# Optimization experiments

Hardware: AMD Instinct MI355X
Metric: run time of the kernel (lower is better)

The kernel has to match this reference:

```python
import jax, jax.numpy as jnp
import numpy as np

B = 256          # graphs per batch
NPG = 512        # nodes per graph (equal-size AIGs)
N = B * NPG      # 131072 total nodes
E = 2 * N        # AIG: ~2 fanins per AND node
H = 256          # hidden_channels
EMB = 3          # node-type embedding dim
IN = EMB + 1     # node_encoder_out_channels


def _p(k, shape, fan_in):
    return jax.random.normal(k, shape, jnp.float32) / np.float32(np.sqrt(fan_in))


def setup_inputs():
    key = jax.random.key(0)
    ks = list(jax.random.split(key, 24))
    nt = jax.random.randint(ks[0], (N, 1), 0, 3)
    ninv = jax.random.randint(ks[1], (N, 1), 0, 3)
    x = jnp.concatenate([nt, ninv], axis=1).astype(jnp.int32)
    # within-graph random edges
    epg = E // B
    gid = jnp.repeat(jnp.arange(B), epg)
    src = gid * NPG + jax.random.randint(ks[2], (E,), 0, NPG)
    dst = gid * NPG + jax.random.randint(ks[3], (E,), 0, NPG)
    edge_index = jnp.stack([src, dst]).astype(jnp.int32)
    batch = jnp.repeat(jnp.arange(B), NPG).astype(jnp.int32)
    d = dict(x=x, edge_index=edge_index, batch=batch)
    d['emb_w'] = _p(ks[4], (3, EMB), 1)
    d['c1_lW'] = _p(ks[5], (IN, H), IN); d['c1_lb'] = jnp.zeros((H,), jnp.float32)
    d['c1_rW'] = _p(ks[6], (IN, H), IN)
    d['t1'] = jnp.float32(0.1)
    d['c2_lW'] = _p(ks[7], (H, H), H); d['c2_lb'] = jnp.zeros((H,), jnp.float32)
    d['c2_rW'] = _p(ks[8], (H, H), H)
    d['t2'] = jnp.float32(0.1)
    d['mlp_W'] = _p(ks[9], (NPG * H, H), NPG * H); d['mlp_b'] = jnp.zeros((H,), jnp.float32)
    d['gru_Wih'] = _p(ks[10], (3 * H, H), H); d['gru_Whh'] = _p(ks[11], (3 * H, H), H)
    d['gru_bih'] = jnp.zeros((3 * H,), jnp.float32); d['gru_bhh'] = jnp.zeros((3 * H,), jnp.float32)
    d['st_Wq'] = _p(ks[12], (3, H, H), H); d['st_bq'] = jnp.zeros((3, H), jnp.float32)
    d['st_Wk'] = _p(ks[13], (3, H, H), H); d['st_bk'] = jnp.zeros((3, H), jnp.float32)
    d['st_Wv'] = _p(ks[14], (3, H, H), H); d['st_bv'] = jnp.zeros((3, H), jnp.float32)
    d['st_Wo'] = _p(ks[15], (3, H, H), H); d['st_bo'] = jnp.zeros((3, H), jnp.float32)
    d['st_lW'] = _p(ks[16], (3, H, H), H); d['st_lb'] = jnp.zeros((3, H), jnp.float32)
    d['pma_lW'] = _p(ks[17], (H, H), H); d['pma_lb'] = jnp.zeros((H,), jnp.float32)
    d['seed'] = _p(ks[18], (1, H), H)
    d['fin_W'] = _p(ks[19], (3 * H, 3 * H), 3 * H); d['fin_b'] = jnp.zeros((3 * H,), jnp.float32)
    return d


def _softmax_aggr(msg, idx, t, n):
    # PyG SoftmaxAggregation: alpha = softmax(msg * t per target segment); sum(msg * alpha)
    logits = msg * t                                   # [E, C]
    m = jax.ops.segment_max(logits, idx, num_segments=n)
    m = jnp.where(jnp.isfinite(m), m, 0.0)             # empty segments -> 0
    ex = jnp.exp(logits - m[idx])
    s = jax.ops.segment_sum(ex, idx, num_segments=n)
    alpha = ex / s[idx]
    return jax.ops.segment_sum(msg * alpha, idx, num_segments=n)


def _sage(h, edge_index, lW, lb, rW, t):
    # SAGEConv: lin_l(softmax_aggr(x_j -> i)) + lin_r(x_i)
    msg = h[edge_index[0]]                             # gather sources [E, C]
    ag = _softmax_aggr(msg, edge_index[1], t, N)       # scatter-softmax-scatter
    return ag @ lW + lb + h @ rW


def _gru_last(xd, Wih, Whh, bih, bhh):
    # torch GRU over [B, T, H]; return last output
    def step(h, x_t):
        gi = x_t @ Wih.T + bih
        gh = h @ Whh.T + bhh
        ir, iz, inn = jnp.split(gi, 3, axis=-1)
        hr, hz, hn = jnp.split(gh, 3, axis=-1)
        r = jax.nn.sigmoid(ir + hr)
        z = jax.nn.sigmoid(iz + hz)
        nn_ = jnp.tanh(inn + r * hn)
        h_new = (1.0 - z) * nn_ + z * h
        return h_new, None
    h0 = jnp.zeros((xd.shape[0], H), xd.dtype)
    hT, _ = jax.lax.scan(step, h0, jnp.swapaxes(xd, 0, 1))
    return hT


def _mab(q, k, Wq, bq, Wk, bk, Wv, bv, Wo, bo, Wl, bl):
    # Set-Transformer MAB, 1 head, no layer norm (PyG defaults)
    Q = q @ Wq + bq
    K = k @ Wk + bk
    V = k @ Wv + bv
    A = jax.nn.softmax(jnp.einsum('bqd,bkd->bqk', Q, K) / np.float32(np.sqrt(H)), axis=-1)
    h = q + (jnp.einsum('bqk,bkd->bqd', A, V) @ Wo + bo)
    return h + jax.nn.relu(h @ Wl + bl)


def _set_transformer(xd, Wq, bq, Wk, bk, Wv, bv, Wo, bo, Wl, bl, pma_lW, pma_lb, seed):
    def mab_i(i, q, k):
        return _mab(q, k, Wq[i], bq[i], Wk[i], bk[i], Wv[i], bv[i], Wo[i], bo[i], Wl[i], bl[i])
    h = mab_i(0, xd, xd)                               # encoder SAB [B, NPG, H]
    kk = jax.nn.relu(h @ pma_lW + pma_lb)
    s = jnp.broadcast_to(seed[None], (xd.shape[0], 1, H))
    s = mab_i(1, s, kk)                                # PMA (1 seed)
    s = mab_i(2, s, s)                                 # decoder SAB
    return s.reshape(xd.shape[0], H)


def _forward(x, edge_index, batch, emb_w, c1_lW, c1_lb, c1_rW, t1, c2_lW, c2_lb, c2_rW, t2,
             mlp_W, mlp_b, gru_Wih, gru_Whh, gru_bih, gru_bhh,
             st_Wq, st_bq, st_Wk, st_bk, st_Wv, st_bv, st_Wo, st_bo, st_lW, st_lb,
             pma_lW, pma_lb, seed, fin_W, fin_b):
    # NodeEncoder: embed node_type, concat num_inverted_predecessors as float
    h = jnp.concatenate([emb_w[x[:, 0]], x[:, 1:2].astype(jnp.float32)], axis=1)  # [N, 4]
    h = jax.nn.relu(_sage(h, edge_index, c1_lW, c1_lb, c1_rW, t1))
    h = jax.nn.relu(_sage(h, edge_index, c2_lW, c2_lb, c2_rW, t2))
    # equal-size sorted graphs -> dense batch is a reshape
    xd = h.reshape(B, NPG, H)
    p1 = xd.reshape(B, NPG * H) @ mlp_W + mlp_b                       # MLPAggregation
    p2 = _gru_last(xd, gru_Wih, gru_Whh, gru_bih, gru_bhh)            # GRUAggregation
    p3 = _set_transformer(xd, st_Wq, st_bq, st_Wk, st_bk, st_Wv, st_bv,
                          st_Wo, st_bo, st_lW, st_lb, pma_lW, pma_lb, seed)
    pooled = jnp.concatenate([p1, p2, p3], axis=1)                    # [B, 3H]
    return pooled @ fin_W + fin_b


def reference(x, edge_index, batch, emb_w, c1_lW, c1_lb, c1_rW, t1, c2_lW, c2_lb, c2_rW, t2,
              mlp_W, mlp_b, gru_Wih, gru_Whh, gru_bih, gru_bhh,
              st_Wq, st_bq, st_Wk, st_bk, st_Wv, st_bv, st_Wo, st_bo, st_lW, st_lb,
              pma_lW, pma_lb, seed, fin_W, fin_b):
    return _forward(x, edge_index, batch, emb_w, c1_lW, c1_lb, c1_rW, t1, c2_lW, c2_lb, c2_rW, t2,
                    mlp_W, mlp_b, gru_Wih, gru_Whh, gru_bih, gru_bhh,
                    st_Wq, st_bq, st_Wk, st_bk, st_Wv, st_bv, st_Wo, st_bo, st_lW, st_lb,
                    pma_lW, pma_lb, seed, fin_W, fin_b)
```

## Files before the change

### kernel.cpp

```cpp
#include <hip/hip_runtime.h>
#include <hip/hip_bf16.h>
#include <math.h>

constexpr int NN   = 131072;
constexpr int NE   = 262144;
constexpr int BG   = 256;

typedef __bf16 bf16x8 __attribute__((ext_vector_type(8)));
typedef float  f32x4  __attribute__((ext_vector_type(4)));
typedef int    i32x4  __attribute__((ext_vector_type(4)));

__device__ inline float sigm(float x){ return 1.f/(1.f+__expf(-x)); }
__device__ inline unsigned short f2bu(float f){
  union{float f;unsigned u;}v; v.f=f;
  unsigned u = v.u + 0x7fffu + ((v.u>>16)&1u);
  return (unsigned short)(u>>16);
}
__device__ inline bf16x8 cvt8(float4 a, float4 b){
  union { ushort u[8]; bf16x8 v; } r;
  r.u[0]=f2bu(a.x); r.u[1]=f2bu(a.y); r.u[2]=f2bu(a.z); r.u[3]=f2bu(a.w);
  r.u[4]=f2bu(b.x); r.u[5]=f2bu(b.y); r.u[6]=f2bu(b.z); r.u[7]=f2bu(b.w);
  return r.v;
}

__global__ void k_zero(int* __restrict__ p, int n){
  int i = blockIdx.x*256 + threadIdx.x;
  if (i < n) p[i] = 0;
}

__global__ void k_node_enc(const int* __restrict__ x, const float* __restrict__ emb,
                           float* __restrict__ h0){
  int n = blockIdx.x*256 + threadIdx.x;
  if (n >= NN) return;
  int nt = x[2*n], ninv = x[2*n+1];
  float4 v; v.x = emb[nt*3+0]; v.y = emb[nt*3+1]; v.z = emb[nt*3+2]; v.w = (float)ninv;
  reinterpret_cast<float4*>(h0)[n] = v;
}

__global__ void k_count(const int* __restrict__ ei, int* __restrict__ deg){
  int e = blockIdx.x*256 + threadIdx.x;
  if (e >= NE) return;
  atomicAdd(&deg[ei[NE + e]], 1);
}
__global__ void k_blocksum(const int* __restrict__ deg, int* __restrict__ bsum){
  __shared__ int sd[256];
  int t = threadIdx.x;
  const int* p = deg + blockIdx.x*1024;
  int s = p[t*4] + p[t*4+1] + p[t*4+2] + p[t*4+3];
  sd[t]=s; __syncthreads();
  for (int d=128; d>0; d>>=1){ if (t<d) sd[t]+=sd[t+d]; __syncthreads(); }
  if (!t) bsum[blockIdx.x] = sd[0];
}
__global__ void k_scanbsum(const int* __restrict__ bsum, int* __restrict__ boff, int* __restrict__ offN){
  __shared__ int s[128];
  int t = threadIdx.x;
  int mine = bsum[t];
  s[t]=mine; __syncthreads();
  for (int d=1; d<128; d<<=1){ int v = (t>=d)? s[t-d]:0; __syncthreads(); s[t]+=v; __syncthreads(); }
  boff[t] = s[t]-mine;
  if (t==127) offN[0] = s[127];
}
__global__ void k_scanchunk(const int* __restrict__ deg, const int* __restrict__ boff, int* __restrict__ offs){
  __shared__ int ts[256];
  int t = threadIdx.x, b = blockIdx.x;
  const int* p = deg + b*1024;
  int v0=p[t*4],v1=p[t*4+1],v2=p[t*4+2],v3=p[t*4+3];
  int mysum=v0+v1+v2+v3;
  ts[t]=mysum; __syncthreads();
  for (int d=1; d<256; d<<=1){ int v=(t>=d)?ts[t-d]:0; __syncthreads(); ts[t]+=v; __syncthreads(); }
  int ex = ts[t]-mysum + boff[b];
  int* o = offs + b*1024 + t*4;
  o[0]=ex; o[1]=ex+v0; o[2]=ex+v0+v1; o[3]=ex+v0+v1+v2;
}
__global__ void k_fill(const int* __restrict__ ei, const int* __restrict__ offs,
                       int* __restrict__ cur, int* __restrict__ esrc){
  int e = blockIdx.x*256 + threadIdx.x;
  if (e >= NE) return;
  int dst = ei[NE+e];
  int pos = offs[dst] + atomicAdd(&cur[dst],1);
  esrc[pos] = ei[e];
}

__global__ void k_aggr4(const float* __restrict__ h, const int* __restrict__ offs,
                        const int* __restrict__ esrc, const float* __restrict__ tptr,
                        float* __restrict__ ag){
  int n = blockIdx.x*256 + threadIdx.x;
  if (n >= NN) return;
  int s = offs[n], e = offs[n+1];
  float4 z = {0,0,0,0};
  if (s == e){ reinterpret_cast<float4*>(ag)[n] = z; return; }
  float t = *tptr;
  float4 num=z, den=z;
  for (int i=s;i<e;++i){
    float4 v = reinterpret_cast<const float4*>(h)[esrc[i]];
    float ex;
    ex=__expf(v.x*t); num.x+=v.x*ex; den.x+=ex;
    ex=__expf(v.y*t); num.y+=v.y*ex; den.y+=ex;
    ex=__expf(v.z*t); num.z+=v.z*ex; den.z+=ex;
    ex=__expf(v.w*t); num.w+=v.w*ex; den.w+=ex;
  }
  float4 r = {num.x/den.x, num.y/den.y, num.z/den.z, num.w/den.w};
  reinterpret_cast<float4*>(ag)[n] = r;
}

__global__ __launch_bounds__(256) void k_aggr256(float* __restrict__ buf, const int* __restrict__ offs,
                          const int* __restrict__ esrc, const float* __restrict__ tptr, int base){
  int n = base + blockIdx.x, c = threadIdx.x;
  int s = offs[n], e = offs[n+1];
  float* outp = buf + (size_t)blockIdx.x*512 + 256 + c;
  if (s == e){ *outp = 0.f; return; }
  float t = *tptr;
  float num=0.f, den=0.f;
  for (int i=s;i<e;++i){
    float v = buf[(size_t)(esrc[i]-base)*512 + c];
    float ex = __expf(v*t);
    num += v*ex; den += ex;
  }
  *outp = num/den;
}

__global__ __launch_bounds__(256) void k_conv1_lin(const float* __restrict__ ag, const float* __restrict__ h0,
                            const float* __restrict__ lW, const float* __restrict__ lb,
                            const float* __restrict__ rW, float* __restrict__ out, int base){
  int n = base + blockIdx.x, c = threadIdx.x;
  float4 a  = reinterpret_cast<const float4*>(ag)[n];
  float4 xv = reinterpret_cast<const float4*>(h0)[n];
  float acc = lb[c];
  acc += a.x*lW[c]  + a.y*lW[256+c]  + a.z*lW[512+c]  + a.w*lW[768+c];
  acc += xv.x*rW[c] + xv.y*rW[256+c] + xv.z*rW[512+c] + xv.w*rW[768+c];
  out[(size_t)blockIdx.x*512 + c] = fmaxf(acc, 0.f);
}

#define GF_BIAS    1
#define GF_RELU    2
#define GF_RESID   4
#define GF_RESID_B 8
#define GF_ADDC    32
#define GF_ATOMIC  64
#define GF_BF16    128
#define GF_VTP     256

__global__ void k_packb(const float* __restrict__ W, ushort* __restrict__ Bp, int K, int N){
  int idx = blockIdx.x*256 + threadIdx.x;
  if (idx >= K*N) return;
  int k = idx / N, j = idx - k*N;
  Bp[((size_t)(k>>3)*N + j)*8 + (k&7)] = f2bu(W[idx]);
}
__global__ void k_packbT(const float* __restrict__ W, ushort* __restrict__ Bp, int K, int N){
  int idx = blockIdx.x*256 + threadIdx.x;
  if (idx >= K*N) return;
  int j = idx / K, k = idx - j*K;
  Bp[((size_t)(k>>3)*N + j)*8 + (k&7)] = f2bu(W[idx]);
}
__global__ __launch_bounds__(256) void k_packhh8(const float* __restrict__ gWhh,
                        char* __restrict__ Bp8, float* __restrict__ cs){
  int j = blockIdx.x, k = threadIdx.x;
  float w = gWhh[(size_t)j*256 + k];
  __shared__ float red[256];
  red[k] = fabsf(w); __syncthreads();
  for (int d=128; d>0; d>>=1){ if (k<d) red[k]=fmaxf(red[k],red[k+d]); __syncthreads(); }
  float mx = fmaxf(red[0], 1e-20f);
  int q = (int)lrintf(w * (127.f/mx));
  q = max(-127, min(127, q));
  Bp8[((size_t)(k>>3)*768 + j)*8 + (k&7)] = (char)q;
  if (k==0) cs[j] = mx/(127.f*127.f);
}
__global__ void k_packbias(const float* __restrict__ gbih, const float* __restrict__ gbhh,
                           float* __restrict__ bc){
  int i = blockIdx.x*256 + threadIdx.x;
  if (i >= 1024) return;
  int c = i & 255;
  float v;
  if (i < 256)      v = gbih[c] + gbhh[c];
  else if (i < 512) v = gbih[256+c] + gbhh[256+c];
  else if (i < 768) v = gbih[512+c];
  else              v = gbhh[512+c];
  bc[i] = v;
}

template<int FLAGS>
__global__ __launch_bounds__(256) void k_bgemm(const float* __restrict__ A, const ushort* __restrict__ Bp,
                       const float* __restrict__ bias, const float* __restrict__ resid,
                       float* __restrict__ C, int M, int Nn, int K, int lda){
  const int tid = threadIdx.x;
  const int wv = tid>>6, lane = tid&63;
  const int mw = wv>>1, nw = wv&1;
  const int arow = lane&15, ks = lane>>4;
  const int m0 = blockIdx.x*128 + mw*64, n0 = blockIdx.y*128 + nw*64;
  const int kChunk = K / gridDim.z, kBeg = blockIdx.z * kChunk;
  f32x4 acc[4][4] = {};
  const float* Arow0 = A + (size_t)(m0 + 0*16 + arow)*lda;
  const float* Arow1 = A + (size_t)(m0 + 1*16 + arow)*lda;
  const float* Arow2 = A + (size_t)(m0 + 2*16 + arow)*lda;
  const float* Arow3 = A + (size_t)(m0 + 3*16 + arow)*lda;
  #pragma unroll 2
  for (int k0 = kBeg; k0 < kBeg+kChunk; k0 += 32){
    const int kb = (k0>>3) + ks;
    bf16x8 af[4];
    {
      const float4* p0 = reinterpret_cast<const float4*>(Arow0 + k0 + ks*8);
      const float4* p1 = reinterpret_cast<const float4*>(Arow1 + k0 + ks*8);
      const float4* p2 = reinterpret_cast<const float4*>(Arow2 + k0 + ks*8);
      const float4* p3 = reinterpret_cast<const float4*>(Arow3 + k0 + ks*8);
      af[0] = cvt8(p0[0], p0[1]);
      af[1] = cvt8(p1[0], p1[1]);
      af[2] = cvt8(p2[0], p2[1]);
      af[3] = cvt8(p3[0], p3[1]);
    }
    #pragma unroll
    for (int nf=0; nf<4; ++nf){
      const int col = n0 + nf*16 + arow;
      bf16x8 bfr = *reinterpret_cast<const bf16x8*>(Bp + ((size_t)kb*Nn + col)*8);
      #pragma unroll
      for (int mf=0; mf<4; ++mf)
        acc[mf][nf] = __builtin_amdgcn_mfma_f32_16x16x32_bf16(af[mf], bfr, acc[mf][nf], 0, 0, 0);
    }
  }
  #pragma unroll
  for (int nf=0; nf<4; ++nf){
    const int n = n0 + nf*16 + arow;
    float bv  = (FLAGS & GF_BIAS)    ? bias[n]  : 0.f;
    float rbv = (FLAGS & GF_RESID_B) ? resid[n] : 0.f;
    #pragma unroll
    for (int mf=0; mf<4; ++mf){
      #pragma unroll
      for (int r=0; r<4; ++r){
        const int m = m0 + mf*16 + ks*4 + r;
        size_t idx = (size_t)m*Nn + n;
        float v = acc[mf][nf][r];
        if (FLAGS & GF_ATOMIC){ atomicAdd(&C[idx], v); }
        else {
          v += bv;
          if (FLAGS & GF_ADDC)  v += C[idx];
          if (FLAGS & GF_RELU)  v = fmaxf(v, 0.f);
          if (FLAGS & GF_RESID) v += resid[idx];
          v += rbv;
          if (FLAGS & GF_VTP){
            const int rr = m & 511, mg = m >> 9;
            ((ushort*)C)[(size_t)mg*131072 + (((rr>>3)*256 + n)<<3) + (rr&7)] = f2bu(v);
          }
          else if (FLAGS & GF_BF16) reinterpret_cast<__hip_bfloat16*>(C)[idx] = __float2bfloat16(v);
          else C[idx] = v;
        }
      }
    }
  }
}

__global__ __launch_bounds__(256) void k_qk(const float* __restrict__ Q, const ushort* __restrict__ Kb,
                                            float* __restrict__ S){
  const int tid = threadIdx.x;
  const int wv = tid>>6, lane = tid&63;
  const int mw = wv>>1, nw = wv&1;
  const int arow = lane&15, ks = lane>>4;
  const int m0 = blockIdx.x*128 + mw*64;
  const int n0 = blockIdx.y*128 + nw*64;
  const int g  = blockIdx.x>>2;
  const ushort* Kg = Kb + (size_t)g*131072;
  f32x4 acc[4][4] = {};
  const float* Ar0 = Q + (size_t)(m0 + 0*16 + arow)*256;
  const float* Ar1 = Q + (size_t)(m0 + 1*16 + arow)*256;
  const float* Ar2 = Q + (size_t)(m0 + 2*16 + arow)*256;
  const float* Ar3 = Q + (size_t)(m0 + 3*16 + arow)*256;
  #pragma unroll
  for (int k0 = 0; k0 < 256; k0 += 32){
    bf16x8 af[4];
    {
      const float4* p0 = reinterpret_cast<const float4*>(Ar0 + k0 + ks*8);
      const float4* p1 = reinterpret_cast<const float4*>(Ar1 + k0 + ks*8);
      const float4* p2 = reinterpret_cast<const float4*>(Ar2 + k0 + ks*8);
      const float4* p3 = reinterpret_cast<const float4*>(Ar3 + k0 + ks*8);
      af[0] = cvt8(p0[0], p0[1]);
      af[1] = cvt8(p1[0], p1[1]);
      af[2] = cvt8(p2[0], p2[1]);
      af[3] = cvt8(p3[0], p3[1]);
    }
    #pragma unroll
    for (int nf=0; nf<4; ++nf){
      const int j = n0 + nf*16 + arow;
      bf16x8 bfr = *reinterpret_cast<const bf16x8*>(Kg + (size_t)j*256 + k0 + ks*8);
      #pragma unroll
      for (int mf=0; mf<4; ++mf)
        acc[mf][nf] = __builtin_amdgcn_mfma_f32_16x16x32_bf16(af[mf], bfr, acc[mf][nf], 0, 0, 0);
    }
  }
  #pragma unroll
  for (int nf=0; nf<4; ++nf){
    const int n = n0 + nf*16 + arow;
    #pragma unroll
    for (int mf=0; mf<4; ++mf){
      #pragma unroll
      for (int r=0; r<4; ++r){
        const int m = m0 + mf*16 + ks*4 + r;
        S[(size_t)m*512 + n] = acc[mf][nf][r];
      }
    }
  }
}

__global__ __launch_bounds__(256) void k_smrow(const float* __restrict__ S, ushort* __restrict__ P){
  const int row = blockIdx.x, tid = threadIdx.x;
  __shared__ float red[4];
  const float* sr = S + (size_t)row*512;
  float s0 = sr[tid], s1 = sr[tid+256];
  float m = fmaxf(s0, s1);
  #pragma unroll
  for (int o=1;o<64;o<<=1) m = fmaxf(m, __shfl_xor(m,o));
  if ((tid&63)==0) red[tid>>6] = m;
  __syncthreads();
  m = fmaxf(fmaxf(red[0],red[1]), fmaxf(red[2],red[3]));
  __syncthreads();
  float e0 = __expf((s0-m)*0.0625f), e1 = __expf((s1-m)*0.0625f);
  float s = e0+e1;
  #pragma unroll
  for (int o=1;o<64;o<<=1) s += __shfl_xor(s,o);
  if ((tid&63)==0) red[tid>>6] = s;
  __syncthreads();
  s = red[0]+red[1]+red[2]+red[3];
  float inv = 1.f/s;
  P[(size_t)row*512 + tid]       = f2bu(e0*inv);
  P[(size_t)row*512 + 256 + tid] = f2bu(e1*inv);
}

__global__ __launch_bounds__(256) void k_av(const ushort* __restrict__ Pb, const ushort* __restrict__ VTp,
                                            float* __restrict__ O){
  const int tid = threadIdx.x;
  const int wv = tid>>6, lane = tid&63;
  const int mw = wv>>1, nw = wv&1;
  const int arow = lane&15, ks = lane>>4;
  const int m0 = blockIdx.x*128 + mw*64;
  const int n0 = blockIdx.y*128 + nw*64;
  const int g  = blockIdx.x>>2;
  const ushort* Vg = VTp + (size_t)g*131072;
  f32x4 acc[4][4] = {};
  const ushort* Pr0 = Pb + (size_t)(m0 + 0*16 + arow)*512;
  const ushort* Pr1 = Pb + (size_t)(m0 + 1*16 + arow)*512;
  const ushort* Pr2 = Pb + (size_t)(m0 + 2*16 + arow)*512;
  const ushort* Pr3 = Pb + (size_t)(m0 + 3*16 + arow)*512;
  #pragma unroll 2
  for (int k0 = 0; k0 < 512; k0 += 32){
    const int kb = (k0>>3) + ks;
    bf16x8 af[4];
    af[0] = *reinterpret_cast<const bf16x8*>(Pr0 + k0 + ks*8);
    af[1] = *reinterpret_cast<const bf16x8*>(Pr1 + k0 + ks*8);
    af[2] = *reinterpret_cast<const bf16x8*>(Pr2 + k0 + ks*8);
    af[3] = *reinterpret_cast<const bf16x8*>(Pr3 + k0 + ks*8);
    #pragma unroll
    for (int nf=0; nf<4; ++nf){
      const int col = n0 + nf*16 + arow;
      bf16x8 bfr = *reinterpret_cast<const bf16x8*>(Vg + ((size_t)kb*256 + col)*8);
      #pragma unroll
      for (int mf=0; mf<4; ++mf)
        acc[mf][nf] = __builtin_amdgcn_mfma_f32_16x16x32_bf16(af[mf], bfr, acc[mf][nf], 0, 0, 0);
    }
  }
  #pragma unroll
  for (int nf=0; nf<4; ++nf){
    const int n = n0 + nf*16 + arow;
    #pragma unroll
    for (int mf=0; mf<4; ++mf){
      #pragma unroll
      for (int r=0; r<4; ++r){
        const int m = m0 + mf*16 + ks*4 + r;
        O[(size_t)m*256 + n] = acc[mf][nf][r];
      }
    }
  }
}

__global__ void k_rowbias(const float* __restrict__ bias, float* __restrict__ C, int Nn, int total){
  int i = blockIdx.x*256 + threadIdx.x;
  if (i < total) C[i] = bias[i % Nn];
}
__global__ void k_qvec(const float* __restrict__ seed, const float* __restrict__ Wq,
                       const float* __restrict__ bq, float* __restrict__ qv){
  __shared__ float s[256];
  int t = threadIdx.x;
  s[t] = seed[t]; __syncthreads();
  float acc = bq[t];
  for (int c = 0; c < 256; ++c) acc += s[c] * Wq[c*256 + t];
  qv[t] = acc;
}
__global__ __launch_bounds__(256) void k_wk2q(const float* __restrict__ Wk2, const float* __restrict__ bk2,
                      const float* __restrict__ qv, float* __restrict__ outv){
  __shared__ float qs[256];
  __shared__ float red[4];
  int t = threadIdx.x;
  qs[t] = qv[t]; __syncthreads();
  float a = 0.f;
  for (int c=0;c<256;c+=4){
    float4 w = *reinterpret_cast<const float4*>(Wk2 + t*256 + c);
    a += w.x*qs[c] + w.y*qs[c+1] + w.z*qs[c+2] + w.w*qs[c+3];
  }
  outv[t] = a;
  float bb = bk2[t]*qs[t];
  #pragma unroll
  for (int o=1;o<64;o<<=1) bb += __shfl_xor(bb,o);
  if ((t&63)==0) red[t>>6] = bb;
  __syncthreads();
  if (t==0) outv[256] = red[0]+red[1]+red[2]+red[3];
}
__global__ __launch_bounds__(256) void k_pmafuse(const float* __restrict__ kk, const float* __restrict__ wkq,
                        float* __restrict__ wsum){
  int g = blockIdx.x, tid = threadIdx.x;
  __shared__ float qs[256];
  __shared__ float sc[512];
  __shared__ float red[4];
  qs[tid] = wkq[tid];
  __syncthreads();
  const float b2q = wkq[256];
  const float* kg = kk + (size_t)g*512*256;
  float l0=0.f, l1=0.f;
  for (int j0=0;j0<2;++j0){
    int j = tid + j0*256;
    const float* kr = kg + (size_t)j*256;
    float a = 0.f;
    for (int c=0;c<256;c+=4){
      float4 k4 = *reinterpret_cast<const float4*>(kr + c);
      a += k4.x*qs[c] + k4.y*qs[c+1] + k4.z*qs[c+2] + k4.w*qs[c+3];
    }
    a = (a + b2q)*0.0625f;
    if (j0) l1=a; else l0=a;
  }
  float m = fmaxf(l0,l1);
  #pragma unroll
  for (int o=1;o<64;o<<=1) m = fmaxf(m, __shfl_xor(m,o));
  if ((tid&63)==0) red[tid>>6] = m;
  __syncthreads();
  m = fmaxf(fmaxf(red[0],red[1]), fmaxf(red[2],red[3]));
  __syncthreads();
  float e0 = __expf(l0-m), e1 = __expf(l1-m);
  sc[tid]=e0; sc[tid+256]=e1;
  float s = e0+e1;
  #pragma unroll
  for (int o=1;o<64;o<<=1) s += __shfl_xor(s,o);
  if ((tid&63)==0) red[tid>>6] = s;
  __syncthreads();
  s = red[0]+red[1]+red[2]+red[3];
  float invs = 1.f/s;
  float acc = 0.f;
  for (int j=0;j<512;++j) acc += sc[j] * kg[(size_t)j*256 + tid];
  wsum[(size_t)g*256+tid] = acc*invs;
}
__global__ void k_concat(const float* __restrict__ p1, const float* __restrict__ p2,
                         const float* __restrict__ p3, float* __restrict__ pooled){
  int idx = blockIdx.x*256 + threadIdx.x;
  int b = idx / 768, j = idx % 768;
  float v = (j < 256) ? p1[b*256+j] : (j < 512) ? p2[b*256+j-256] : p3[b*256+j-512];
  pooled[idx] = v;
}

__global__ __launch_bounds__(512) void k_gru10(const float* __restrict__ X,
                      const ushort* __restrict__ pIh, const char* __restrict__ pHh8,
                      const float* __restrict__ csg, const float* __restrict__ bc,
                      float* __restrict__ p2){
  extern __shared__ char gsm[];
  float*  GIw  = (float*)gsm;
  float*  gh   = (float*)(gsm + 98304);
  float*  bcl  = (float*)(gsm + 101376);
  float*  csl  = (float*)(gsm + 105472);
  char*   hbf8 = (char*) (gsm + 108544);
  const int g = blockIdx.x;
  const int tid = threadIdx.x;
  const int wv = tid>>6, lane = tid&63;
  const int arow = lane&15, ks = lane>>4;
  for (int i=tid;i<1024;i+=512) bcl[i] = bc[i];
  for (int i=tid;i<768;i+=512)  csl[i] = csg[i];
  if (tid < 256) hbf8[tid] = 0;
  float h_reg = 0.f;
  const float* Xg = X + (size_t)g*512*256;
  __syncthreads();
  for (int w=0; w<16; ++w){
    const int t0 = w*32;
    #pragma unroll
    for (int mt=0; mt<2; ++mt){
      const float* xr = Xg + (size_t)(t0 + mt*16 + arow)*256;
      f32x4 acc[6] = {};
      #pragma unroll
      for (int kt=0; kt<8; ++kt){
        const float4* xp = reinterpret_cast<const float4*>(xr + kt*32 + ks*8);
        bf16x8 af = cvt8(xp[0], xp[1]);
        #pragma unroll
        for (int nt=0; nt<6; ++nt){
          bf16x8 bfr = *reinterpret_cast<const bf16x8*>(pIh + ((size_t)(kt*4+ks)*768 + wv*96+nt*16+arow)*8);
          acc[nt] = __builtin_amdgcn_mfma_f32_16x16x32_bf16(af, bfr, acc[nt], 0,0,0);
        }
      }
      #pragma unroll
      for (int nt=0; nt<6; ++nt){
        const int col = wv*96 + nt*16 + arow;
        #pragma unroll
        for (int r=0;r<4;++r)
          GIw[(size_t)(mt*16 + ks*4 + r)*768 + col] = acc[nt][r];
      }
    }
    for (int dt=0; dt<32; ++dt){
      i32x4 sacc[6] = {};
      #pragma unroll
      for (int kt=0; kt<8; ++kt){
        long a8 = 0;
        if (arow == 0) a8 = *reinterpret_cast<const long*>(hbf8 + kt*32 + ks*8);
        #pragma unroll
        for (int nt=0; nt<6; ++nt){
          const int col = wv*96 + nt*16 + arow;
          long b8 = *reinterpret_cast<const long*>(pHh8 + ((size_t)(kt*4+ks)*768 + col)*8);
          sacc[nt] = __builtin_amdgcn_mfma_i32_16x16x32_i8(a8, b8, sacc[nt], 0,0,0);
        }
      }
      if (ks == 0){
        #pragma unroll
        for (int nt=0; nt<6; ++nt){
          const int col = wv*96 + nt*16 + arow;
          gh[col] = (float)sacc[nt][0] * csl[col];
        }
      }
      __syncthreads();
      if (tid < 256){
        const int c = tid;
        const float* gir = GIw + (size_t)dt*768;
        float rr = sigm(gir[c]     + gh[c]     + bcl[c]);
        float zz = sigm(gir[256+c] + gh[256+c] + bcl[256+c]);
        float nn = tanhf(gir[512+c] + bcl[512+c] + rr*(gh[512+c] + bcl[768+c]));
        h_reg = (1.f-zz)*nn + zz*h_reg;
        int q = (int)lrintf(h_reg*127.f);
        q = max(-127, min(127, q));
        hbf8[c] = (char)q;
      }
      __syncthreads();
    }
  }
  if (tid < 256) p2[(size_t)g*256 + tid] = h_reg;
}

extern "C" void kernel_launch(void* const* d_in, const int* in_sizes, int n_in,
                              void* d_out, int out_size, void* d_ws, size_t ws_size,
                              hipStream_t stream){
  const int*   x      = (const int*)  d_in[0];
  const int*   ei     = (const int*)  d_in[1];
  const float* emb_w  = (const float*)d_in[3];
  const float* c1_lW  = (const float*)d_in[4];
  const float* c1_lb  = (const float*)d_in[5];
  const float* c1_rW  = (const float*)d_in[6];
  const float* t1     = (const float*)d_in[7];
  const float* c2_lW  = (const float*)d_in[8];
  const float* c2_lb  = (const float*)d_in[9];
  const float* c2_rW  = (const float*)d_in[10];
  const float* t2     = (const float*)d_in[11];
  const float* mlp_W  = (const float*)d_in[12];
  const float* mlp_b  = (const float*)d_in[13];
  const float* gWih   = (const float*)d_in[14];
  const float* gWhh   = (const float*)d_in[15];
  const float* gbih   = (const float*)d_in[16];
  const float* gbhh   = (const float*)d_in[17];
  const float* stWq   = (const float*)d_in[18];
  const float* stbq   = (const float*)d_in[19];
  const float* stWk   = (const float*)d_in[20];
  const float* stbk   = (const float*)d_in[21];
  const float* stWv   = (const float*)d_in[22];
  const float* stbv   = (const float*)d_in[23];
  const float* stWo   = (const float*)d_in[24];
  const float* stbo   = (const float*)d_in[25];
  const float* stlW   = (const float*)d_in[26];
  const float* stlb   = (const float*)d_in[27];
  const float* pma_lW = (const float*)d_in[28];
  const float* pma_lb = (const float*)d_in[29];
  const float* seed   = (const float*)d_in[30];
  const float* fin_W  = (const float*)d_in[31];
  const float* fin_b  = (const float*)d_in[32];
  float* out = (float*)d_out;

  auto needFor = [](int CHe)->size_t{
    size_t bufN = (size_t)CHe*512*512;
    size_t floats = (size_t)33554432 + 3*bufN + 2*524288 + 2*196608 + 8*65536 + 196608 + 320 + 512;
    size_t ints   = 131072 + 131200 + 131072 + 262144 + 128 + 128;
    return floats*4 + ints*4 + 4096;
  };
  const int CHe = (ws_size >= needFor(64)) ? 64 : 32;
  if (ws_size < needFor(32)) return;
  const int NCHUNKe = BG / CHe;
  const int NCNe = CHe * 512;
  const size_t bufN = (size_t)CHe*512*512;

  float* H2   = (float*)d_ws;
  float* bufA = H2   + (size_t)33554432;
  float* bufB = bufA + bufN;
  float* bufC = bufB + bufN;
  float* h0   = bufC + bufN;
  float* ag1  = h0   + (size_t)524288;
  float* wT1  = ag1  + (size_t)524288;
  float* wT2  = wT1  + (size_t)196608;
  float* p1   = wT2  + (size_t)196608;
  float* p2   = p1   + (size_t)65536;
  float* p3   = p2   + (size_t)65536;
  float* av2  = p3   + (size_t)65536;
  float* s1   = av2  + (size_t)65536;
  float* s2v  = s1   + (size_t)65536;
  float* v3   = s2v  + (size_t)65536;
  float* h3   = v3   + (size_t)65536;
  float* pooled = h3 + (size_t)65536;
  float* qv   = pooled + (size_t)196608;
  int*   deg  = (int*)(qv + 320);
  int*   offs = deg  + 131072;
  int*   cur  = offs + 131200;
  int*   esrc = cur  + 131072;
  int*   bsum = esrc + 262144;
  int*   boff = bsum + 128;
  float* wkq  = (float*)(boff + 128);

  ushort* pIh  = (ushort*)wT1;
  char*   pHh8 = (char*)(wT1 + 98304);
  float*  csHh = wT1 + 98304 + 49152;
  ushort* pC2  = (ushort*)wT2;
  float*  bcomb= wT2 + 65536;
  float*  pa   = h0;
  ushort* pQ0  = (ushort*)(pa);
  ushort* pK0  = (ushort*)(pa + 32768);
  ushort* pV0  = (ushort*)(pa + 65536);
  ushort* pO0  = (ushort*)(pa + 98304);
  ushort* pL0  = (ushort*)(pa + 131072);
  ushort* pPma = (ushort*)(pa + 163840);
  ushort* pV1  = (ushort*)(pa + 229376);
  ushort* pO1  = (ushort*)(pa + 262144);
  ushort* pL1  = (ushort*)(pa + 294912);
  ushort* pV2  = (ushort*)(pa + 327680);
  ushort* pO2  = (ushort*)(pa + 360448);
  ushort* pL2  = (ushort*)(pa + 393216);
  ushort* pFin = (ushort*)(pa + 425984);

  ushort* VTp = (ushort*)(bufA + bufN/2);
  ushort* Kbf = (ushort*)bufB;
  ushort* Pbf = (ushort*)(bufB + bufN/4);

  const int ls0 = 65536, ls1 = 256;

  k_node_enc<<<NN/256, 256, 0, stream>>>(x, emb_w, h0);

  k_zero<<<NN/256, 256, 0, stream>>>(deg, NN);
  k_count<<<NE/256, 256, 0, stream>>>(ei, deg);
  k_blocksum<<<128, 256, 0, stream>>>(deg, bsum);
  k_scanbsum<<<1, 128, 0, stream>>>(bsum, boff, offs + NN);
  k_scanchunk<<<128, 256, 0, stream>>>(deg, boff, offs);
  k_zero<<<NN/256, 256, 0, stream>>>(cur, NN);
  k_fill<<<NE/256, 256, 0, stream>>>(ei, offs, cur, esrc);

  k_aggr4<<<NN/256, 256, 0, stream>>>(h0, offs, esrc, t1, ag1);
  k_packb <<<256, 256, 0, stream>>>(c2_rW, pC2, 256, 256);
  k_packb <<<256, 256, 0, stream>>>(c2_lW, pC2 + 65536, 256, 256);
  k_packbT<<<768, 256, 0, stream>>>(gWih, pIh, 256, 768);
  k_packhh8<<<768, 256, 0, stream>>>(gWhh, pHh8, csHh);
  k_packbias<<<4, 256, 0, stream>>>(gbih, gbhh, bcomb);

  for (int cg = 0; cg < NCHUNKe; ++cg){
    const int base = cg * NCNe;
    float* Hc = H2 + (size_t)base * 256;
    const dim3 gg(NCNe/128, 2, 1);
    k_conv1_lin<<<NCNe, 256, 0, stream>>>(ag1, h0, c1_lW, c1_lb, c1_rW, bufA, base);
    k_aggr256<<<NCNe, 256, 0, stream>>>(bufA, offs, esrc, t2, base);
    k_bgemm<GF_BIAS|GF_RELU><<<gg, 256, 0, stream>>>(bufA, pC2, c2_lb, nullptr, Hc, NCNe, 256, 512, 512);
  }

  k_packb<<<131072, 256, 0, stream>>>(mlp_W, (ushort*)bufB, 131072, 256);
  k_rowbias<<<256, 256, 0, stream>>>(mlp_b, p1, 256, 65536);
  k_bgemm<GF_ATOMIC><<<dim3(2, 2, 64), 256, 0, stream>>>(H2, (ushort*)bufB, nullptr, nullptr, p1, 256, 256, NN, 131072);

  k_gru10<<<BG, 512, 108800, stream>>>(H2, pIh, pHh8, csHh, bcomb, p2);

  k_packb<<<256, 256, 0, stream>>>(stWq,        pQ0, 256, 256);
  k_packb<<<256, 256, 0, stream>>>(stWk,        pK0, 256, 256);
  k_packb<<<256, 256, 0, stream>>>(stWv,        pV0, 256, 256);
  k_packb<<<256, 256, 0, stream>>>(stWo,        pO0, 256, 256);
  k_packb<<<256, 256, 0, stream>>>(stlW,        pL0, 256, 256);
  k_packb<<<256, 256, 0, stream>>>(pma_lW,      pPma,256, 256);
  k_packb<<<256, 256, 0, stream>>>(stWv + ls0,  pV1, 256, 256);
  k_packb<<<256, 256, 0, stream>>>(stWo + ls0,  pO1, 256, 256);
  k_packb<<<256, 256, 0, stream>>>(stlW + ls0,  pL1, 256, 256);
  k_packb<<<256, 256, 0, stream>>>(stWv + 2*ls0,pV2, 256, 256);
  k_packb<<<256, 256, 0, stream>>>(stWo + 2*ls0,pO2, 256, 256);
  k_packb<<<256, 256, 0, stream>>>(stlW + 2*ls0,pL2, 256, 256);
  k_packb<<<2304, 256, 0, stream>>>(fin_W,      pFin,768, 768);
  k_qvec<<<1, 256, 0, stream>>>(seed, stWq + ls0, stbq + ls1, qv);
  k_wk2q<<<1, 256, 0, stream>>>(stWk + ls0, stbk + ls1, qv, wkq);

  for (int cg = 0; cg < NCHUNKe; ++cg){
    const int base = cg * NCNe;
    float* Hc = H2 + (size_t)base * 256;
    const dim3 gg(NCNe/128, 2, 1);
    k_bgemm<GF_BIAS><<<gg, 256, 0, stream>>>(Hc, pQ0, stbq, nullptr, bufA, NCNe, 256, 256, 256);
    k_bgemm<GF_BIAS|GF_BF16><<<gg, 256, 0, stream>>>(Hc, pK0, stbk, nullptr, (float*)Kbf, NCNe, 256, 256, 256);
    k_bgemm<GF_BIAS|GF_VTP><<<gg, 256, 0, stream>>>(Hc, pV0, stbv, nullptr, (float*)VTp, NCNe, 256, 256, 256);
    k_qk<<<dim3(NCNe/128, 4), 256, 0, stream>>>(bufA, Kbf, bufC);
    k_smrow<<<NCNe, 256, 0, stream>>>(bufC, Pbf);
    k_av<<<dim3(NCNe/128, 2), 256, 0, stream>>>(Pbf, VTp, bufA);
    k_bgemm<GF_BIAS|GF_RESID><<<gg, 256, 0, stream>>>(bufA, pO0, stbo, Hc, Hc, NCNe, 256, 256, 256);
    k_bgemm<GF_BIAS|GF_RELU|GF_RESID><<<gg, 256, 0, stream>>>(Hc, pL0, stlb, Hc, bufA, NCNe, 256, 256, 256);
    k_bgemm<GF_BIAS|GF_RELU><<<gg, 256, 0, stream>>>(bufA, pPma, pma_lb, nullptr, bufB, NCNe, 256, 256, 256);
    k_pmafuse<<<CHe, 256, 0, stream>>>(bufB, wkq, av2 + (size_t)cg*CHe*256);
  }

  k_bgemm<GF_BIAS><<<dim3(2, 2, 1), 256, 0, stream>>>(av2, pV1, stbv + ls1, nullptr, v3, 256, 256, 256, 256);
  k_bgemm<GF_BIAS|GF_RESID_B><<<dim3(2, 2, 1), 256, 0, stream>>>(v3, pO1, stbo + ls1, seed, s1, 256, 256, 256, 256);
  k_bgemm<GF_BIAS|GF_RELU|GF_RESID><<<dim3(2, 2, 1), 256, 0, stream>>>(s1, pL1, stlb + ls1, s1, s2v, 256, 256, 256, 256);
  k_bgemm<GF_BIAS><<<dim3(2, 2, 1), 256, 0, stream>>>(s2v, pV2, stbv + 2*ls1, nullptr, v3, 256, 256, 256, 256);
  k_bgemm<GF_BIAS|GF_RESID><<<dim3(2, 2, 1), 256, 0, stream>>>(v3, pO2, stbo + 2*ls1, s2v, h3, 256, 256, 256, 256);
  k_bgemm<GF_BIAS|GF_RELU|GF_RESID><<<dim3(2, 2, 1), 256, 0, stream>>>(h3, pL2, stlb + 2*ls1, h3, p3, 256, 256, 256, 256);

  k_concat<<<768, 256, 0, stream>>>(p1, p2, p3, pooled);
  k_bgemm<GF_BIAS><<<dim3(2, 6, 1), 256, 0, stream>>>(pooled, pFin, fin_b, nullptr, out, 256, 768, 768, 768);
}
```

Before: 3.152 ms.

## Store node activations and attention intermediates in bf16, widen GEMM tiles

The conv2 output H2 and the set-transformer intermediates (Q, attention output, residual stream, PMA keys) are now stored as bf16 instead of fp32. Downstream GEMMs load bf16 fragments directly instead of converting fp32, and the GRU, MLP split-K and PMA kernels read bf16 too. A new GEMM kernel covers all 256 output columns per block with wider N tiles, and GRU tanh is replaced by an exp-based fast form. This halves activation memory traffic and conversion work, at the cost of extra rounding, since the residual stream is now accumulated in bf16.

```diff
diff --git a/kernel.cpp b/kernel.cpp
--- a/kernel.cpp
+++ b/kernel.cpp
@@ -11,6 +11,9 @@
 typedef int    i32x4  __attribute__((ext_vector_type(4)));
 
 __device__ inline float sigm(float x){ return 1.f/(1.f+__expf(-x)); }
+__device__ inline float blo(unsigned u){ union{unsigned a;float f;}v; v.a=u<<16; return v.f; }
+__device__ inline float bhi(unsigned u){ union{unsigned a;float f;}v; v.a=u&0xffff0000u; return v.f; }
+__device__ inline float b2f(ushort u){ union{unsigned a;float f;}v; v.a=((unsigned)u)<<16; return v.f; }
 __device__ inline unsigned short f2bu(float f){
   union{float f;unsigned u;}v; v.f=f;
   unsigned u = v.u + 0x7fffu + ((v.u>>16)&1u);
@@ -139,6 +142,7 @@
 #define GF_ATOMIC  64
 #define GF_BF16    128
 #define GF_VTP     256
+#define GF_RESID16 512
 
 __global__ void k_packb(const float* __restrict__ W, ushort* __restrict__ Bp, int K, int N){
   int idx = blockIdx.x*256 + threadIdx.x;
@@ -187,25 +191,15 @@
   const int mw = wv>>1, nw = wv&1;
   const int arow = lane&15, ks = lane>>4;
   const int m0 = blockIdx.x*128 + mw*64, n0 = blockIdx.y*128 + nw*64;
-  const int kChunk = K / gridDim.z, kBeg = blockIdx.z * kChunk;
   f32x4 acc[4][4] = {};
-  const float* Arow0 = A + (size_t)(m0 + 0*16 + arow)*lda;
-  const float* Arow1 = A + (size_t)(m0 + 1*16 + arow)*lda;
-  const float* Arow2 = A + (size_t)(m0 + 2*16 + arow)*lda;
-  const float* Arow3 = A + (size_t)(m0 + 3*16 + arow)*lda;
   #pragma unroll 2
-  for (int k0 = kBeg; k0 < kBeg+kChunk; k0 += 32){
+  for (int k0 = 0; k0 < K; k0 += 32){
     const int kb = (k0>>3) + ks;
     bf16x8 af[4];
-    {
-      const float4* p0 = reinterpret_cast<const float4*>(Arow0 + k0 + ks*8);
-      const float4* p1 = reinterpret_cast<const float4*>(Arow1 + k0 + ks*8);
-      const float4* p2 = reinterpret_cast<const float4*>(Arow2 + k0 + ks*8);
-      const float4* p3 = reinterpret_cast<const float4*>(Arow3 + k0 + ks*8);
-      af[0] = cvt8(p0[0], p0[1]);
-      af[1] = cvt8(p1[0], p1[1]);
-      af[2] = cvt8(p2[0], p2[1]);
-      af[3] = cvt8(p3[0], p3[1]);
+    #pragma unroll
+    for (int mf=0; mf<4; ++mf){
+      const float4* p = reinterpret_cast<const float4*>(A + (size_t)(m0+mf*16+arow)*lda + k0 + ks*8);
+      af[mf] = cvt8(p[0], p[1]);
     }
     #pragma unroll
     for (int nf=0; nf<4; ++nf){
@@ -228,27 +222,86 @@
         const int m = m0 + mf*16 + ks*4 + r;
         size_t idx = (size_t)m*Nn + n;
         float v = acc[mf][nf][r];
-        if (FLAGS & GF_ATOMIC){ atomicAdd(&C[idx], v); }
+        v += bv;
+        if (FLAGS & GF_RELU)  v = fmaxf(v, 0.f);
+        if (FLAGS & GF_RESID) v += resid[idx];
+        v += rbv;
+        C[idx] = v;
+      }
+    }
+  }
+}
+
+template<int FLAGS, bool ABF>
+__global__ __launch_bounds__(256) void k_bgemm2(const void* __restrict__ Av, const ushort* __restrict__ Bp,
+                       const float* __restrict__ bias, const void* __restrict__ residv,
+                       void* __restrict__ Cv, int K, int lda){
+  const int tid = threadIdx.x;
+  const int wv = tid>>6, lane = tid&63;
+  const int mw = wv&1, nw = wv>>1;
+  const int arow = lane&15, ks = lane>>4;
+  const int m0 = blockIdx.x*128 + mw*64;
+  const int n0 = nw*128;
+  const int kChunk = K / gridDim.z, kBeg = blockIdx.z * kChunk;
+  f32x4 acc[4][8] = {};
+  #pragma unroll 1
+  for (int k0 = kBeg; k0 < kBeg+kChunk; k0 += 32){
+    const int kb = (k0>>3) + ks;
+    bf16x8 af[4];
+    if (ABF){
+      const ushort* A = (const ushort*)Av;
+      #pragma unroll
+      for (int mf=0; mf<4; ++mf)
+        af[mf] = *reinterpret_cast<const bf16x8*>(A + (size_t)(m0+mf*16+arow)*lda + k0 + ks*8);
+    } else {
+      const float* A = (const float*)Av;
+      #pragma unroll
+      for (int mf=0; mf<4; ++mf){
+        const float4* p = reinterpret_cast<const float4*>(A + (size_t)(m0+mf*16+arow)*lda + k0 + ks*8);
+        af[mf] = cvt8(p[0], p[1]);
+      }
+    }
+    #pragma unroll
+    for (int nf=0; nf<8; ++nf){
+      const int col = n0 + nf*16 + arow;
+      bf16x8 bfr = *reinterpret_cast<const bf16x8*>(Bp + ((size_t)kb*256 + col)*8);
+      #pragma unroll
+      for (int mf=0; mf<4; ++mf)
+        acc[mf][nf] = __builtin_amdgcn_mfma_f32_16x16x32_bf16(af[mf], bfr, acc[mf][nf], 0, 0, 0);
+    }
+  }
+  #pragma unroll
+  for (int nf=0; nf<8; ++nf){
+    const int n = n0 + nf*16 + arow;
+    float bv = (FLAGS & GF_BIAS) ? bias[n] : 0.f;
+    #pragma unroll
+    for (int mf=0; mf<4; ++mf){
+      #pragma unroll
+      for (int r=0; r<4; ++r){
+        const int m = m0 + mf*16 + ks*4 + r;
+        size_t idx = (size_t)m*256 + n;
+        float v = acc[mf][nf][r];
+        if (FLAGS & GF_ATOMIC){ atomicAdd((float*)Cv + idx, v); }
         else {
           v += bv;
-          if (FLAGS & GF_ADDC)  v += C[idx];
-          if (FLAGS & GF_RELU)  v = fmaxf(v, 0.f);
-          if (FLAGS & GF_RESID) v += resid[idx];
-          v += rbv;
+          if (FLAGS & GF_RELU) v = fmaxf(v, 0.f);
+          if (FLAGS & GF_RESID16) v += b2f(((const ushort*)residv)[idx]);
           if (FLAGS & GF_VTP){
             const int rr = m & 511, mg = m >> 9;
-            ((ushort*)C)[(size_t)mg*131072 + (((rr>>3)*256 + n)<<3) + (rr&7)] = f2bu(v);
+            ((ushort*)Cv)[(size_t)mg*131072 + (((rr>>3)*256 + n)<<3) + (rr&7)] = f2bu(v);
+          } else if (FLAGS & GF_BF16){
+            ((ushort*)Cv)[idx] = f2bu(v);
+          } else {
+            ((float*)Cv)[idx] = v;
           }
-          else if (FLAGS & GF_BF16) reinterpret_cast<__hip_bfloat16*>(C)[idx] = __float2bfloat16(v);
-          else C[idx] = v;
         }
       }
     }
   }
 }
 
-__global__ __launch_bounds__(256) void k_qk(const float* __restrict__ Q, const ushort* __restrict__ Kb,
-                                            float* __restrict__ S){
+__global__ __launch_bounds__(256) void k_qk16(const ushort* __restrict__ Qb, const ushort* __restrict__ Kb,
+                                              float* __restrict__ S){
   const int tid = threadIdx.x;
   const int wv = tid>>6, lane = tid&63;
   const int mw = wv>>1, nw = wv&1;
@@ -258,23 +311,12 @@
   const int g  = blockIdx.x>>2;
   const ushort* Kg = Kb + (size_t)g*131072;
   f32x4 acc[4][4] = {};
-  const float* Ar0 = Q + (size_t)(m0 + 0*16 + arow)*256;
-  const float* Ar1 = Q + (size_t)(m0 + 1*16 + arow)*256;
-  const float* Ar2 = Q + (size_t)(m0 + 2*16 + arow)*256;
-  const float* Ar3 = Q + (size_t)(m0 + 3*16 + arow)*256;
   #pragma unroll
   for (int k0 = 0; k0 < 256; k0 += 32){
     bf16x8 af[4];
-    {
-      const float4* p0 = reinterpret_cast<const float4*>(Ar0 + k0 + ks*8);
-      const float4* p1 = reinterpret_cast<const float4*>(Ar1 + k0 + ks*8);
-      const float4* p2 = reinterpret_cast<const float4*>(Ar2 + k0 + ks*8);
-      const float4* p3 = reinterpret_cast<const float4*>(Ar3 + k0 + ks*8);
-      af[0] = cvt8(p0[0], p0[1]);
-      af[1] = cvt8(p1[0], p1[1]);
-      af[2] = cvt8(p2[0], p2[1]);
-      af[3] = cvt8(p3[0], p3[1]);
-    }
+    #pragma unroll
+    for (int mf=0; mf<4; ++mf)
+      af[mf] = *reinterpret_cast<const bf16x8*>(Qb + (size_t)(m0+mf*16+arow)*256 + k0 + ks*8);
     #pragma unroll
     for (int nf=0; nf<4; ++nf){
       const int j = n0 + nf*16 + arow;
@@ -322,31 +364,26 @@
   P[(size_t)row*512 + 256 + tid] = f2bu(e1*inv);
 }
 
-__global__ __launch_bounds__(256) void k_av(const ushort* __restrict__ Pb, const ushort* __restrict__ VTp,
-                                            float* __restrict__ O){
+__global__ __launch_bounds__(256) void k_av2(const ushort* __restrict__ Pb, const ushort* __restrict__ VTp,
+                                             ushort* __restrict__ Ob){
   const int tid = threadIdx.x;
   const int wv = tid>>6, lane = tid&63;
-  const int mw = wv>>1, nw = wv&1;
+  const int mw = wv&1, nw = wv>>1;
   const int arow = lane&15, ks = lane>>4;
   const int m0 = blockIdx.x*128 + mw*64;
-  const int n0 = blockIdx.y*128 + nw*64;
+  const int n0 = nw*128;
   const int g  = blockIdx.x>>2;
   const ushort* Vg = VTp + (size_t)g*131072;
-  f32x4 acc[4][4] = {};
-  const ushort* Pr0 = Pb + (size_t)(m0 + 0*16 + arow)*512;
-  const ushort* Pr1 = Pb + (size_t)(m0 + 1*16 + arow)*512;
-  const ushort* Pr2 = Pb + (size_t)(m0 + 2*16 + arow)*512;
-  const ushort* Pr3 = Pb + (size_t)(m0 + 3*16 + arow)*512;
-  #pragma unroll 2
+  f32x4 acc[4][8] = {};
+  #pragma unroll 1
   for (int k0 = 0; k0 < 512; k0 += 32){
     const int kb = (k0>>3) + ks;
     bf16x8 af[4];
-    af[0] = *reinterpret_cast<const bf16x8*>(Pr0 + k0 + ks*8);
-    af[1] = *reinterpret_cast<const bf16x8*>(Pr1 + k0 + ks*8);
-    af[2] = *reinterpret_cast<const bf16x8*>(Pr2 + k0 + ks*8);
-    af[3] = *reinterpret_cast<const bf16x8*>(Pr3 + k0 + ks*8);
-    #pragma unroll
-    for (int nf=0; nf<4; ++nf){
+    #pragma unroll
+    for (int mf=0; mf<4; ++mf)
+      af[mf] = *reinterpret_cast<const bf16x8*>(Pb + (size_t)(m0+mf*16+arow)*512 + k0 + ks*8);
+    #pragma unroll
+    for (int nf=0; nf<8; ++nf){
       const int col = n0 + nf*16 + arow;
       bf16x8 bfr = *reinterpret_cast<const bf16x8*>(Vg + ((size_t)kb*256 + col)*8);
       #pragma unroll
@@ -355,14 +392,14 @@
     }
   }
   #pragma unroll
-  for (int nf=0; nf<4; ++nf){
+  for (int nf=0; nf<8; ++nf){
     const int n = n0 + nf*16 + arow;
     #pragma unroll
     for (int mf=0; mf<4; ++mf){
       #pragma unroll
       for (int r=0; r<4; ++r){
         const int m = m0 + mf*16 + ks*4 + r;
-        O[(size_t)m*256 + n] = acc[mf][nf][r];
+        Ob[(size_t)m*256 + n] = f2bu(acc[mf][nf][r]);
       }
     }
   }
@@ -400,7 +437,7 @@
   __syncthreads();
   if (t==0) outv[256] = red[0]+red[1]+red[2]+red[3];
 }
-__global__ __launch_bounds__(256) void k_pmafuse(const float* __restrict__ kk, const float* __restrict__ wkq,
+__global__ __launch_bounds__(256) void k_pmafuse16(const ushort* __restrict__ kkb, const float* __restrict__ wkq,
                         float* __restrict__ wsum){
   int g = blockIdx.x, tid = threadIdx.x;
   __shared__ float qs[256];
@@ -409,15 +446,17 @@
   qs[tid] = wkq[tid];
   __syncthreads();
   const float b2q = wkq[256];
-  const float* kg = kk + (size_t)g*512*256;
+  const ushort* kg = kkb + (size_t)g*512*256;
   float l0=0.f, l1=0.f;
   for (int j0=0;j0<2;++j0){
     int j = tid + j0*256;
-    const float* kr = kg + (size_t)j*256;
+    const ushort* kr = kg + (size_t)j*256;
     float a = 0.f;
-    for (int c=0;c<256;c+=4){
-      float4 k4 = *reinterpret_cast<const float4*>(kr + c);
-      a += k4.x*qs[c] + k4.y*qs[c+1] + k4.z*qs[c+2] + k4.w*qs[c+3];
+    for (int c8=0;c8<32;++c8){
+      uint4 kv = *reinterpret_cast<const uint4*>(kr + c8*8);
+      const float* qq = qs + c8*8;
+      a += qq[0]*blo(kv.x)+qq[1]*bhi(kv.x)+qq[2]*blo(kv.y)+qq[3]*bhi(kv.y)
+         + qq[4]*blo(kv.z)+qq[5]*bhi(kv.z)+qq[6]*blo(kv.w)+qq[7]*bhi(kv.w);
     }
     a = (a + b2q)*0.0625f;
     if (j0) l1=a; else l0=a;
@@ -439,7 +478,7 @@
   s = red[0]+red[1]+red[2]+red[3];
   float invs = 1.f/s;
   float acc = 0.f;
-  for (int j=0;j<512;++j) acc += sc[j] * kg[(size_t)j*256 + tid];
+  for (int j=0;j<512;++j) acc += sc[j] * b2f(kg[(size_t)j*256 + tid]);
   wsum[(size_t)g*256+tid] = acc*invs;
 }
 __global__ void k_concat(const float* __restrict__ p1, const float* __restrict__ p2,
@@ -450,7 +489,7 @@
   pooled[idx] = v;
 }
 
-__global__ __launch_bounds__(512) void k_gru10(const float* __restrict__ X,
+__global__ __launch_bounds__(512) void k_gru12(const ushort* __restrict__ X,
                       const ushort* __restrict__ pIh, const char* __restrict__ pHh8,
                       const float* __restrict__ csg, const float* __restrict__ bc,
                       float* __restrict__ p2){
@@ -468,18 +507,17 @@
   for (int i=tid;i<768;i+=512)  csl[i] = csg[i];
   if (tid < 256) hbf8[tid] = 0;
   float h_reg = 0.f;
-  const float* Xg = X + (size_t)g*512*256;
+  const ushort* Xg = X + (size_t)g*512*256;
   __syncthreads();
   for (int w=0; w<16; ++w){
     const int t0 = w*32;
     #pragma unroll
     for (int mt=0; mt<2; ++mt){
-      const float* xr = Xg + (size_t)(t0 + mt*16 + arow)*256;
+      const ushort* xr = Xg + (size_t)(t0 + mt*16 + arow)*256;
       f32x4 acc[6] = {};
       #pragma unroll
       for (int kt=0; kt<8; ++kt){
-        const float4* xp = reinterpret_cast<const float4*>(xr + kt*32 + ks*8);
-        bf16x8 af = cvt8(xp[0], xp[1]);
+        bf16x8 af = *reinterpret_cast<const bf16x8*>(xr + kt*32 + ks*8);
         #pragma unroll
         for (int nt=0; nt<6; ++nt){
           bf16x8 bfr = *reinterpret_cast<const bf16x8*>(pIh + ((size_t)(kt*4+ks)*768 + wv*96+nt*16+arow)*8);
@@ -520,7 +558,10 @@
         const float* gir = GIw + (size_t)dt*768;
         float rr = sigm(gir[c]     + gh[c]     + bcl[c]);
         float zz = sigm(gir[256+c] + gh[256+c] + bcl[256+c]);
-        float nn = tanhf(gir[512+c] + bcl[512+c] + rr*(gh[512+c] + bcl[768+c]));
+        float nx = gir[512+c] + bcl[512+c] + rr*(gh[512+c] + bcl[768+c]);
+        nx = fminf(fmaxf(nx, -15.f), 15.f);
+        float e2 = __expf(2.f*nx);
+        float nn = (e2-1.f)*__builtin_amdgcn_rcpf(e2+1.f);
         h_reg = (1.f-zz)*nn + zz*h_reg;
         int q = (int)lrintf(h_reg*127.f);
         q = max(-127, min(127, q));
@@ -607,6 +648,7 @@
   int*   boff = bsum + 128;
   float* wkq  = (float*)(boff + 128);
 
+  ushort* H2b  = (ushort*)H2;
   ushort* pIh  = (ushort*)wT1;
   char*   pHh8 = (char*)(wT1 + 98304);
   float*  csHh = wT1 + 98304 + 49152;
@@ -627,9 +669,13 @@
   ushort* pL2  = (ushort*)(pa + 393216);
   ushort* pFin = (ushort*)(pa + 425984);
 
+  ushort* Qbf = (ushort*)bufA;
+  ushort* Obf = (ushort*)(bufA + bufN/4);
   ushort* VTp = (ushort*)(bufA + bufN/2);
   ushort* Kbf = (ushort*)bufB;
   ushort* Pbf = (ushort*)(bufB + bufN/4);
+  ushort* Ebf = Qbf;
+  ushort* kkb = Kbf;
 
   const int ls0 = 65536, ls1 = 256;
 
@@ -652,18 +698,17 @@
 
   for (int cg = 0; cg < NCHUNKe; ++cg){
     const int base = cg * NCNe;
-    float* Hc = H2 + (size_t)base * 256;
-    const dim3 gg(NCNe/128, 2, 1);
+    ushort* Hcb = H2b + (size_t)base * 256;
     k_conv1_lin<<<NCNe, 256, 0, stream>>>(ag1, h0, c1_lW, c1_lb, c1_rW, bufA, base);
     k_aggr256<<<NCNe, 256, 0, stream>>>(bufA, offs, esrc, t2, base);
-    k_bgemm<GF_BIAS|GF_RELU><<<gg, 256, 0, stream>>>(bufA, pC2, c2_lb, nullptr, Hc, NCNe, 256, 512, 512);
+    k_bgemm2<GF_BIAS|GF_RELU|GF_BF16, false><<<NCNe/128, 256, 0, stream>>>(bufA, pC2, c2_lb, nullptr, Hcb, 512, 512);
   }
 
   k_packb<<<131072, 256, 0, stream>>>(mlp_W, (ushort*)bufB, 131072, 256);
   k_rowbias<<<256, 256, 0, stream>>>(mlp_b, p1, 256, 65536);
-  k_bgemm<GF_ATOMIC><<<dim3(2, 2, 64), 256, 0, stream>>>(H2, (ushort*)bufB, nullptr, nullptr, p1, 256, 256, NN, 131072);
-
-  k_gru10<<<BG, 512, 108800, stream>>>(H2, pIh, pHh8, csHh, bcomb, p2);
+  k_bgemm2<GF_ATOMIC, true><<<dim3(2, 1, 128), 256, 0, stream>>>(H2b, (ushort*)bufB, nullptr, nullptr, p1, NN, 131072);
+
+  k_gru12<<<BG, 512, 108800, stream>>>(H2b, pIh, pHh8, csHh, bcomb, p2);
 
   k_packb<<<256, 256, 0, stream>>>(stWq,        pQ0, 256, 256);
   k_packb<<<256, 256, 0, stream>>>(stWk,        pK0, 256, 256);
@@ -683,18 +728,18 @@
 
   for (int cg = 0; cg < NCHUNKe; ++cg){
     const int base = cg * NCNe;
-    float* Hc = H2 + (size_t)base * 256;
-    const dim3 gg(NCNe/128, 2, 1);
-    k_bgemm<GF_BIAS><<<gg, 256, 0, stream>>>(Hc, pQ0, stbq, nullptr, bufA, NCNe, 256, 256, 256);
-    k_bgemm<GF_BIAS|GF_BF16><<<gg, 256, 0, stream>>>(Hc, pK0, stbk, nullptr, (float*)Kbf, NCNe, 256, 256, 256);
-    k_bgemm<GF_BIAS|GF_VTP><<<gg, 256, 0, stream>>>(Hc, pV0, stbv, nullptr, (float*)VTp, NCNe, 256, 256, 256);
-    k_qk<<<dim3(NCNe/128, 4), 256, 0, stream>>>(bufA, Kbf, bufC);
+    ushort* Hcb = H2b + (size_t)base * 256;
+    const int gb1 = NCNe/128;
+    k_bgemm2<GF_BIAS|GF_BF16, true><<<gb1, 256, 0, stream>>>(Hcb, pQ0, stbq, nullptr, Qbf, 256, 256);
+    k_bgemm2<GF_BIAS|GF_BF16, true><<<gb1, 256, 0, stream>>>(Hcb, pK0, stbk, nullptr, Kbf, 256, 256);
+    k_bgemm2<GF_BIAS|GF_VTP,  true><<<gb1, 256, 0, stream>>>(Hcb, pV0, stbv, nullptr, VTp, 256, 256);
+    k_qk16<<<dim3(gb1, 4), 256, 0, stream>>>(Qbf, Kbf, bufC);
     k_smrow<<<NCNe, 256, 0, stream>>>(bufC, Pbf);
-    k_av<<<dim3(NCNe/128, 2), 256, 0, stream>>>(Pbf, VTp, bufA);
-    k_bgemm<GF_BIAS|GF_RESID><<<gg, 256, 0, stream>>>(bufA, pO0, stbo, Hc, Hc, NCNe, 256, 256, 256);
-    k_bgemm<GF_BIAS|GF_RELU|GF_RESID><<<gg, 256, 0, stream>>>(Hc, pL0, stlb, Hc, bufA, NCNe, 256, 256, 256);
-    k_bgemm<GF_BIAS|GF_RELU><<<gg, 256, 0, stream>>>(bufA, pPma, pma_lb, nullptr, bufB, NCNe, 256, 256, 256);
-    k_pmafuse<<<CHe, 256, 0, stream>>>(bufB, wkq, av2 + (size_t)cg*CHe*256);
+    k_av2<<<gb1, 256, 0, stream>>>(Pbf, VTp, Obf);
+    k_bgemm2<GF_BIAS|GF_RESID16|GF_BF16, true><<<gb1, 256, 0, stream>>>(Obf, pO0, stbo, Hcb, Hcb, 256, 256);
+    k_bgemm2<GF_BIAS|GF_RELU|GF_RESID16|GF_BF16, true><<<gb1, 256, 0, stream>>>(Hcb, pL0, stlb, Hcb, Ebf, 256, 256);
+    k_bgemm2<GF_BIAS|GF_RELU|GF_BF16, true><<<gb1, 256, 0, stream>>>(Ebf, pPma, pma_lb, nullptr, kkb, 256, 256);
+    k_pmafuse16<<<CHe, 256, 0, stream>>>(kkb, wkq, av2 + (size_t)cg*CHe*256);
   }
 
   k_bgemm<GF_BIAS><<<dim3(2, 2, 1), 256, 0, stream>>>(av2, pV1, stbv + ls1, nullptr, v3, 256, 256, 256, 256);
```

Measured after the change: 2.732 ms. 1.15x faster.
